# Kernel optimization log

Hardware: AMD Instinct MI355X
Metric: run time of the kernel (lower is better)

## Reference

```python
import jax, jax.numpy as jnp
import numpy as np

N = 50000          # nodes
E_RAND = 800000    # random edges
E = E_RAND + N     # + self loops -> 850000
F_IN = 256         # nembed
F_HID = 64         # nhid
H = 8              # nheads
NCLASS = 40
ALPHA = 0.2        # leakyrelu slope


def setup_inputs() -> dict:
    key = jax.random.key(0)
    ks = jax.random.split(key, 8)
    x = jax.random.normal(ks[0], (N, F_IN), dtype=jnp.float32)
    # random edges + self loops (guarantees every row-sum > 0, like adj + I)
    er = jax.random.randint(ks[1], (2, E_RAND), 0, N, dtype=jnp.int32)
    loops = jnp.tile(jnp.arange(N, dtype=jnp.int32)[None, :], (2, 1))
    edge_index = jnp.concatenate([er, loops], axis=1)  # [2, E]
    # per-head attention params (xavier-ish scale)
    W = jax.random.normal(ks[2], (H, F_IN, F_HID), dtype=jnp.float32) * (1.0 / np.sqrt(F_IN))
    a = jax.random.normal(ks[3], (H, 2 * F_HID), dtype=jnp.float32) * 0.1
    Wo = jax.random.normal(ks[4], (H * F_HID, F_HID), dtype=jnp.float32) * (1.0 / np.sqrt(H * F_HID))
    ao = jax.random.normal(ks[5], (2 * F_HID,), dtype=jnp.float32) * 0.1
    mlp_w = jax.random.normal(ks[6], (NCLASS, F_HID), dtype=jnp.float32) * 0.05
    mlp_b = jnp.zeros((NCLASS,), dtype=jnp.float32)
    return {"x": x, "edge_index": edge_index, "W": W, "a": a,
            "Wo": Wo, "ao": ao, "mlp_w": mlp_w, "mlp_b": mlp_b}


def _leaky(v):
    return jnp.where(v > 0, v, ALPHA * v)


def _spgat_layer(x, W, a, src, dst, n):
    """pyGAT SpGraphAttentionLayer (eval mode, dropout = identity).
    out[i] = sum_{e: src=i} exp(-leakyrelu(a.[h_src;h_dst])) * h[dst] / rowsum_i
    """
    h = x @ W                         # [N, D]
    D = W.shape[1]
    s_src = h @ a[:D]                 # [N]
    s_dst = h @ a[D:]                 # [N]
    # per-edge unnormalized attention (note the -exp(leaky) of original sp impl)
    e = jnp.exp(-_leaky(s_src[src] + s_dst[dst]))          # [E]
    rowsum = jax.ops.segment_sum(e, src, num_segments=n)   # [N]
    num = jax.ops.segment_sum(e[:, None] * h[dst], src, num_segments=n)  # [N, D]
    return num / rowsum[:, None]


def reference(x, edge_index, W, a, Wo, ao, mlp_w, mlp_b):
    src, dst = edge_index[0], edge_index[1]
    # multi-head attention, concat=True -> elu inside each head
    heads = [jax.nn.elu(_spgat_layer(x, W[i], a[i], src, dst, N)) for i in range(H)]
    xc = jnp.concatenate(heads, axis=1)                     # [N, H*F_HID]
    # dropout (eval) = identity
    xo = jax.nn.elu(_spgat_layer(xc, Wo, ao, src, dst, N))  # [N, F_HID]
    return xo @ mlp_w.T + mlp_b                             # [N, NCLASS]
```

## Files before the change

kernel.cpp:

```cpp
#include <hip/hip_runtime.h>

#define NN 50000
#define HH 8
#define ALPHA 0.2f
#define NPAD 50048

typedef short short8 __attribute__((ext_vector_type(8)));
typedef float f32x4 __attribute__((ext_vector_type(4)));

__device__ __forceinline__ float elu_f(float x) {
  return x > 0.f ? x : __expf(x) - 1.f;
}

__device__ __forceinline__ unsigned short f2bf(float f) {
  unsigned int u = __float_as_uint(f);
  unsigned int r = (u + 0x7fffu + ((u >> 16) & 1u)) >> 16;
  return (unsigned short)r;
}

__global__ void cvt_w_kernel(const float* __restrict__ W, unsigned short* __restrict__ Wt,
                             const float* __restrict__ Wo, unsigned short* __restrict__ Wot) {
  int tid = blockIdx.x * 256 + threadIdx.x;
  if (tid < HH * 256 * 64) {
    int h = tid / (256 * 64);
    int rem = tid - h * 256 * 64;
    int k = rem >> 6, c = rem & 63;
    Wt[((size_t)h * 64 + c) * 256 + k] = f2bf(W[tid]);
    return;
  }
  int t2 = tid - HH * 256 * 64;
  if (t2 < 512 * 64) {
    int k = t2 >> 6, c = t2 & 63;
    Wot[(size_t)c * 512 + k] = f2bf(Wo[t2]);
  }
}

__global__ void hist_kernel(const int* __restrict__ src, int* __restrict__ cnt, int E) {
  int e = blockIdx.x * blockDim.x + threadIdx.x;
  if (e < E) atomicAdd(&cnt[src[e]], 1);
}

__global__ __launch_bounds__(1024) void scan_blocks_kernel(const int* __restrict__ cnt,
    int* __restrict__ tmp, int* __restrict__ bsum, int n) {
  __shared__ int sh[1024];
  int i = blockIdx.x * 1024 + threadIdx.x;
  int v = (i < n) ? cnt[i] : 0;
  sh[threadIdx.x] = v;
  __syncthreads();
  for (int off = 1; off < 1024; off <<= 1) {
    int t = (threadIdx.x >= off) ? sh[threadIdx.x - off] : 0;
    __syncthreads();
    sh[threadIdx.x] += t;
    __syncthreads();
  }
  if (i < n) tmp[i] = sh[threadIdx.x] - v;
  if (threadIdx.x == 1023) bsum[blockIdx.x] = sh[1023];
}

__global__ __launch_bounds__(1024) void scan_apply_kernel(const int* __restrict__ tmp,
    const int* __restrict__ bsum, int* __restrict__ row_ptr, int* __restrict__ nxt,
    int n, int E, int nb) {
  __shared__ int boff_sh;
  if (threadIdx.x < 64) {
    int L = threadIdx.x;
    int v = (L < nb && L < (int)blockIdx.x) ? bsum[L] : 0;
#pragma unroll
    for (int off = 1; off < 64; off <<= 1) v += __shfl_xor(v, off, 64);
    if (L == 0) boff_sh = v;
  }
  __syncthreads();
  int i = blockIdx.x * 1024 + threadIdx.x;
  if (i < n) {
    int s = tmp[i] + boff_sh;
    row_ptr[i] = s;
    nxt[i] = s;
  }
  if (i == 0) row_ptr[n] = E;
}

__global__ void scatter_kernel(const int* __restrict__ src, const int* __restrict__ dst,
                               int* __restrict__ nxt, int* __restrict__ col, int E) {
  int e = blockIdx.x * blockDim.x + threadIdx.x;
  if (e < E) {
    int p = atomicAdd(&nxt[src[e]], 1);
    col[p] = dst[e];
  }
}

__global__ __launch_bounds__(256) void mfma_gemm1_kernel(
    const float* __restrict__ X, const unsigned short* __restrict__ Bt,
    const float* __restrict__ Aatt, unsigned short* __restrict__ Cout,
    float* __restrict__ ss, float* __restrict__ sd, int N) {
  __shared__ unsigned short Bs[64][264];
  unsigned short* stage = &Bs[0][0];
  int w = threadIdx.x >> 6, L = threadIdx.x & 63;
  int quad = L >> 4, l16 = L & 15;
  int m0 = blockIdx.x * 64;
  int myrow = m0 + w * 16 + l16;
  int rowc = min(myrow, N - 1);

  const float* Ar = X + (size_t)rowc * 256 + quad * 8;
  short8 areg[8];
#pragma unroll
  for (int ks = 0; ks < 8; ++ks) {
    float4 a0 = *(const float4*)(Ar + ks * 32);
    float4 a1 = *(const float4*)(Ar + ks * 32 + 4);
    areg[ks][0] = (short)f2bf(a0.x); areg[ks][1] = (short)f2bf(a0.y);
    areg[ks][2] = (short)f2bf(a0.z); areg[ks][3] = (short)f2bf(a0.w);
    areg[ks][4] = (short)f2bf(a1.x); areg[ks][5] = (short)f2bf(a1.y);
    areg[ks][6] = (short)f2bf(a1.z); areg[ks][7] = (short)f2bf(a1.w);
  }

  for (int y = 0; y < HH; ++y) {
    __syncthreads();
    {
      const unsigned short* Bsrc = Bt + (size_t)y * 64 * 256;
      for (int c = threadIdx.x; c < 2048; c += 256) {
        int n = c >> 5;
        int kq = (c & 31) << 3;
        *(uint4*)&Bs[n][kq] = *(const uint4*)(Bsrc + (size_t)n * 256 + kq);
      }
    }
    __syncthreads();

    f32x4 acc[4];
#pragma unroll
    for (int nt = 0; nt < 4; ++nt) acc[nt] = (f32x4)(0.f);
#pragma unroll
    for (int ks = 0; ks < 8; ++ks) {
#pragma unroll
      for (int nt = 0; nt < 4; ++nt) {
        short8 b = *(const short8*)&Bs[l16 + 16 * nt][ks * 32 + quad * 8];
        acc[nt] = __builtin_amdgcn_mfma_f32_16x16x32_bf16(areg[ks], b, acc[nt], 0, 0, 0);
      }
    }

    float as[4], ad[4];
#pragma unroll
    for (int nt = 0; nt < 4; ++nt) {
      as[nt] = Aatt[y * 128 + l16 + 16 * nt];
      ad[nt] = Aatt[y * 128 + 64 + l16 + 16 * nt];
    }
#pragma unroll
    for (int reg = 0; reg < 4; ++reg) {
      float p = 0.f, q = 0.f;
#pragma unroll
      for (int nt = 0; nt < 4; ++nt) {
        p += acc[nt][reg] * as[nt];
        q += acc[nt][reg] * ad[nt];
      }
#pragma unroll
      for (int off = 1; off < 16; off <<= 1) {
        p += __shfl_xor(p, off, 64);
        q += __shfl_xor(q, off, 64);
      }
      int row = m0 + w * 16 + quad * 4 + reg;
      if (l16 == 0 && row < N) {
        ss[(size_t)row * 8 + y] = p;
        sd[(size_t)row * 8 + y] = q;
      }
    }

    __syncthreads();
#pragma unroll
    for (int reg = 0; reg < 4; ++reg) {
      int lrow = w * 16 + quad * 4 + reg;
#pragma unroll
      for (int nt = 0; nt < 4; ++nt)
        stage[lrow * 72 + l16 + 16 * nt] = f2bf(acc[nt][reg]);
    }
    __syncthreads();
#pragma unroll
    for (int i = 0; i < 2; ++i) {
      int idx = threadIdx.x + 256 * i;
      int row = idx >> 3;
      int c8 = (idx & 7) << 3;
      if (m0 + row < N) {
        uint4 v = *(const uint4*)&stage[row * 72 + c8];
        *(uint4*)(Cout + ((size_t)(m0 + row)) * 512 + y * 64 + c8) = v;
      }
    }
  }
}

__global__ __launch_bounds__(256) void mfma_gemm2_kernel(
    const unsigned short* __restrict__ A, const unsigned short* __restrict__ Bt,
    const float* __restrict__ Aatt, unsigned short* __restrict__ Cout,
    float* __restrict__ ss, float* __restrict__ sd, int N) {
  __shared__ unsigned short Bs[64][520];
  unsigned short* stage = &Bs[0][0];
  {
    for (int c = threadIdx.x; c < 4096; c += 256) {
      int n = c >> 6;
      int kq = (c & 63) << 3;
      *(uint4*)&Bs[n][kq] = *(const uint4*)(Bt + (size_t)n * 512 + kq);
    }
  }
  __syncthreads();

  int w = threadIdx.x >> 6, L = threadIdx.x & 63;
  int quad = L >> 4, l16 = L & 15;
  int m0 = blockIdx.x * 64;
  int myrow = m0 + w * 16 + l16;
  const unsigned short* Ar = A + (size_t)myrow * 512 + quad * 8;

  f32x4 acc[4];
#pragma unroll
  for (int nt = 0; nt < 4; ++nt) acc[nt] = (f32x4)(0.f);

  short8 a_cur = *(const short8*)(Ar);
  for (int k0 = 0; k0 < 512; k0 += 32) {
    short8 a_nxt;
    if (k0 + 32 < 512) a_nxt = *(const short8*)(Ar + k0 + 32);
#pragma unroll
    for (int nt = 0; nt < 4; ++nt) {
      short8 b = *(const short8*)&Bs[l16 + 16 * nt][k0 + quad * 8];
      acc[nt] = __builtin_amdgcn_mfma_f32_16x16x32_bf16(a_cur, b, acc[nt], 0, 0, 0);
    }
    a_cur = a_nxt;
  }

  float as[4], ad[4];
#pragma unroll
  for (int nt = 0; nt < 4; ++nt) {
    as[nt] = Aatt[l16 + 16 * nt];
    ad[nt] = Aatt[64 + l16 + 16 * nt];
  }
#pragma unroll
  for (int reg = 0; reg < 4; ++reg) {
    float p = 0.f, q = 0.f;
#pragma unroll
    for (int nt = 0; nt < 4; ++nt) {
      p += acc[nt][reg] * as[nt];
      q += acc[nt][reg] * ad[nt];
    }
#pragma unroll
    for (int off = 1; off < 16; off <<= 1) {
      p += __shfl_xor(p, off, 64);
      q += __shfl_xor(q, off, 64);
    }
    int row = m0 + w * 16 + quad * 4 + reg;
    if (l16 == 0 && row < N) { ss[row] = p; sd[row] = q; }
  }

  __syncthreads();
#pragma unroll
  for (int reg = 0; reg < 4; ++reg) {
    int lrow = w * 16 + quad * 4 + reg;
#pragma unroll
    for (int nt = 0; nt < 4; ++nt)
      stage[lrow * 72 + l16 + 16 * nt] = f2bf(acc[nt][reg]);
  }
  __syncthreads();
#pragma unroll
  for (int i = 0; i < 2; ++i) {
    int idx = threadIdx.x + 256 * i;
    int row = idx >> 3;
    int c8 = (idx & 7) << 3;
    if (m0 + row < N) {
      uint4 v = *(const uint4*)&stage[row * 72 + c8];
      *(uint4*)(Cout + ((size_t)(m0 + row)) * 64 + c8) = v;
    }
  }
}

__global__ __launch_bounds__(256) void agg1_kernel(const unsigned short* __restrict__ table,
    const float* __restrict__ ss, const float* __restrict__ sd,
    const int* __restrict__ row_ptr, const int* __restrict__ col,
    unsigned short* __restrict__ xc, int N) {
  int bid = blockIdx.x;
  int r8 = bid & 7;
  int p = r8 >> 2;
  int nb = ((bid >> 3) << 2) | (r8 & 3);
  int wid = threadIdx.x >> 6, L = threadIdx.x & 63;
  int n = nb * 4 + wid;
  if (n >= N) return;
  int hq = L >> 4;
  int h = p * 4 + hq;
  int el = L & 15;
  float ssn = ss[n * 8 + h];
  int k0 = row_ptr[n], deg = row_ptr[n + 1] - k0;
  float acc[4] = {0.f, 0.f, 0.f, 0.f};
  float rs = 0.f;
  const char* tb = (const char*)table + p * 512;

  for (int c0 = 0; c0 < deg; c0 += 64) {
    int j = c0 + L;
    int d_l = (j < deg) ? col[k0 + j] : 0;
    int m = min(64, deg - c0);
    for (int g = 0; g < m; g += 16) {
      int eoff = g + el;
      int de = __shfl(d_l, eoff, 64);
      float s = ssn + sd[(size_t)de * 8 + h];
      float e = __expf(-fmaxf(s, ALPHA * s));
      if (eoff >= m) e = 0.f;
      rs += e;
      int gm = min(16, m - g);
      uint2 rv[16];
#pragma unroll
      for (int t = 0; t < 16; ++t) {
        if (t < gm) {
          int dg = __builtin_amdgcn_readlane(d_l, g + t);
          rv[t] = *(const uint2*)(tb + (size_t)dg * 1024 + L * 8);
        }
      }
#pragma unroll
      for (int t = 0; t < 16; ++t) {
        if (t < gm) {
          float ew = __shfl(e, (hq << 4) + t, 64);
          acc[0] += ew * __uint_as_float(rv[t].x << 16);
          acc[1] += ew * __uint_as_float(rv[t].x & 0xffff0000u);
          acc[2] += ew * __uint_as_float(rv[t].y << 16);
          acc[3] += ew * __uint_as_float(rv[t].y & 0xffff0000u);
        }
      }
    }
  }
  rs += __shfl_xor(rs, 1, 64);
  rs += __shfl_xor(rs, 2, 64);
  rs += __shfl_xor(rs, 4, 64);
  rs += __shfl_xor(rs, 8, 64);
  float inv = 1.f / rs;
  ushort4 pk;
  pk.x = f2bf(elu_f(acc[0] * inv));
  pk.y = f2bf(elu_f(acc[1] * inv));
  pk.z = f2bf(elu_f(acc[2] * inv));
  pk.w = f2bf(elu_f(acc[3] * inv));
  *(ushort4*)(xc + (size_t)n * 512 + p * 256 + L * 4) = pk;
}

__global__ __launch_bounds__(256) void agg2_final_kernel(const unsigned short* __restrict__ table,
    const float* __restrict__ ss, const float* __restrict__ sd,
    const int* __restrict__ row_ptr, const int* __restrict__ col,
    const float* __restrict__ mlp_w, const float* __restrict__ mlp_b,
    float* __restrict__ out, int N) {
  __shared__ float wsh[40 * 65];
  __shared__ float bsh[40];
  __shared__ float osh[4][68];
  for (int i = threadIdx.x; i < 40 * 64; i += 256) wsh[(i >> 6) * 65 + (i & 63)] = mlp_w[i];
  if (threadIdx.x < 40) bsh[threadIdx.x] = mlp_b[threadIdx.x];
  __syncthreads();

  int wid = threadIdx.x >> 6, L = threadIdx.x & 63;
  int n = blockIdx.x * 4 + wid;
  bool act = (n < N);
  float o = 0.f;
  if (act) {
    float ssn = ss[n];
    int k0 = row_ptr[n], deg = row_ptr[n + 1] - k0;
    float acc = 0.f, rs = 0.f;
    const char* base = (const char*)table;
    for (int c0 = 0; c0 < deg; c0 += 64) {
      int j = c0 + L;
      int d_l = 0;
      float e_l = 0.f;
      if (j < deg) {
        d_l = col[k0 + j];
        float s = ssn + sd[d_l];
        e_l = __expf(-fmaxf(s, ALPHA * s));
      }
      rs += e_l;
      int m = min(64, deg - c0);
      int off_l = d_l << 7;
      for (int g = 0; g < m; g += 8) {
        int gm = min(8, m - g);
        unsigned hv[8];
#pragma unroll
        for (int t = 0; t < 8; ++t) {
          if (t < gm) {
            int so = __builtin_amdgcn_readlane(off_l, g + t);
            hv[t] = *(const unsigned short*)(base + so + L * 2);
          }
        }
#pragma unroll
        for (int t = 0; t < 8; ++t) {
          if (t < gm) {
            float ew = __uint_as_float(
                (unsigned)__builtin_amdgcn_readlane(__float_as_uint(e_l), g + t));
            acc += ew * __uint_as_float(hv[t] << 16);
          }
        }
      }
    }
#pragma unroll
    for (int off = 1; off < 64; off <<= 1) rs += __shfl_xor(rs, off, 64);
    o = elu_f(acc / rs);
  }
  osh[wid][L] = o;
  __syncthreads();
  if (act && L < 40) {
    const float* wr = wsh + L * 65;
    const float* orow = osh[wid];
    float acc = bsh[L];
#pragma unroll
    for (int j = 0; j < 64; ++j) acc += orow[j] * wr[j];
    out[(size_t)n * 40 + L] = acc;
  }
}

extern "C" void kernel_launch(void* const* d_in, const int* in_sizes, int n_in,
                              void* d_out, int out_size, void* d_ws, size_t ws_size,
                              hipStream_t stream) {
  (void)n_in; (void)out_size; (void)ws_size;
  const float* x  = (const float*)d_in[0];
  const int*   ei = (const int*)d_in[1];
  const float* W  = (const float*)d_in[2];
  const float* a  = (const float*)d_in[3];
  const float* Wo = (const float*)d_in[4];
  const float* ao = (const float*)d_in[5];
  const float* mw = (const float*)d_in[6];
  const float* mb = (const float*)d_in[7];
  float* out = (float*)d_out;

  const int N = NN;
  const int E = in_sizes[1] / 2;
  const int* src = ei;
  const int* dst = ei + E;

  char* ws = (char*)d_ws;
  size_t off = 0;
  auto alloc = [&](size_t bytes) {
    char* p = ws + off;
    off = (off + bytes + 255) & ~(size_t)255;
    return p;
  };
  unsigned short* Wt  = (unsigned short*)alloc((size_t)HH * 64 * 256 * 2);
  unsigned short* Wot = (unsigned short*)alloc((size_t)64 * 512 * 2);
  unsigned short* h1b = (unsigned short*)alloc((size_t)N * 512 * 2);
  float* ss1     = (float*)alloc((size_t)N * 8 * 4);
  float* sd1     = (float*)alloc((size_t)N * 8 * 4);
  unsigned short* xc = (unsigned short*)alloc((size_t)NPAD * 512 * 2);
  unsigned short* h2b = (unsigned short*)alloc((size_t)N * 64 * 2);
  float* ss2     = (float*)alloc((size_t)N * 4);
  float* sd2     = (float*)alloc((size_t)N * 4);
  int*   row_ptr = (int*)  alloc((size_t)(N + 1) * 4);
  int*   nxt     = (int*)  alloc((size_t)N * 4);
  int*   cnt     = (int*)  alloc((size_t)N * 4);
  int*   tmp     = (int*)  alloc((size_t)N * 4);
  int*   bsum    = (int*)  alloc(64 * 4);
  int*   colv    = (int*)  alloc((size_t)E * 4);

  int eb = (E + 255) / 256;
  int nb1024 = (N + 1023) / 1024;

  hipLaunchKernelGGL(cvt_w_kernel, dim3((HH * 256 * 64 + 512 * 64 + 255) / 256), dim3(256),
                     0, stream, W, Wt, Wo, Wot);

  hipMemsetAsync(cnt, 0, (size_t)N * 4, stream);
  hipLaunchKernelGGL(hist_kernel, dim3(eb), dim3(256), 0, stream, src, cnt, E);
  hipLaunchKernelGGL(scan_blocks_kernel, dim3(nb1024), dim3(1024), 0, stream, cnt, tmp, bsum, N);
  hipLaunchKernelGGL(scan_apply_kernel, dim3(nb1024), dim3(1024), 0, stream,
                     tmp, bsum, row_ptr, nxt, N, E, nb1024);
  hipLaunchKernelGGL(scatter_kernel, dim3(eb), dim3(256), 0, stream, src, dst, nxt, colv, E);

  hipLaunchKernelGGL(mfma_gemm1_kernel, dim3(NPAD / 64), dim3(256), 0, stream,
                     x, Wt, a, h1b, ss1, sd1, N);
  hipLaunchKernelGGL(agg1_kernel, dim3(2 * ((N + 3) / 4)), dim3(256), 0, stream,
                     h1b, ss1, sd1, row_ptr, colv, xc, N);

  hipLaunchKernelGGL(mfma_gemm2_kernel, dim3(NPAD / 64), dim3(256), 0, stream,
                     xc, Wot, ao, h2b, ss2, sd2, N);
  hipLaunchKernelGGL(agg2_final_kernel, dim3((N + 3) / 4), dim3(256), 0, stream,
                     h2b, ss2, sd2, row_ptr, colv, mw, mb, out, N);
}
```

Before: 444.4 us.

## Pre-convert x to bf16 and retile GEMM1 as 128x128 block tiles

Adds a combined conversion kernel that writes x to a padded bf16 buffer and lays out W and Wo transposed in bf16. GEMM1 becomes a 2D-grid 128x128 tiled MFMA kernel with a k-loop through shared memory, each wave computing a 64x64 subtile of one head. The intent is higher MFMA density and register reuse per block. In exchange it adds an extra pass over x, drops the staged vectorized output stores for scattered 2-byte stores, and synchronizes every k-step.

Result: faster. 432.8 us (-2.6%).

```diff
diff --git a/kernel.cpp b/kernel.cpp
--- a/kernel.cpp
+++ b/kernel.cpp
@@ -18,20 +18,35 @@
   return (unsigned short)r;
 }
 
-__global__ void cvt_w_kernel(const float* __restrict__ W, unsigned short* __restrict__ Wt,
-                             const float* __restrict__ Wo, unsigned short* __restrict__ Wot) {
+__global__ void cvt_all_kernel(const float* __restrict__ x, unsigned short* __restrict__ xb,
+                               const float* __restrict__ W, unsigned short* __restrict__ Wtc,
+                               const float* __restrict__ Wo, unsigned short* __restrict__ Wot,
+                               int N) {
   int tid = blockIdx.x * 256 + threadIdx.x;
-  if (tid < HH * 256 * 64) {
-    int h = tid / (256 * 64);
-    int rem = tid - h * 256 * 64;
-    int k = rem >> 6, c = rem & 63;
-    Wt[((size_t)h * 64 + c) * 256 + k] = f2bf(W[tid]);
+  int n4x = NPAD * 64;
+  if (tid < n4x) {
+    int row = tid >> 6;
+    ushort4 o;
+    if (row < N) {
+      float4 v = ((const float4*)x)[tid];
+      o.x = f2bf(v.x); o.y = f2bf(v.y); o.z = f2bf(v.z); o.w = f2bf(v.w);
+    } else {
+      o.x = o.y = o.z = o.w = 0;
+    }
+    ((ushort4*)xb)[tid] = o;
     return;
   }
-  int t2 = tid - HH * 256 * 64;
-  if (t2 < 512 * 64) {
-    int k = t2 >> 6, c = t2 & 63;
-    Wot[(size_t)c * 512 + k] = f2bf(Wo[t2]);
+  int t1 = tid - n4x;
+  if (t1 < 512 * 256) {
+    int c = t1 >> 8, k = t1 & 255;
+    int h = c >> 6, cc = c & 63;
+    Wtc[t1] = f2bf(W[((size_t)h * 256 + k) * 64 + cc]);
+    return;
+  }
+  int t2 = t1 - 512 * 256;
+  if (t2 < 64 * 512) {
+    int c = t2 >> 9, k = t2 & 511;
+    Wot[t2] = f2bf(Wo[(size_t)k * 64 + c]);
   }
 }
 
@@ -88,96 +103,79 @@
 }
 
 __global__ __launch_bounds__(256) void mfma_gemm1_kernel(
-    const float* __restrict__ X, const unsigned short* __restrict__ Bt,
+    const unsigned short* __restrict__ A, const unsigned short* __restrict__ Wtc,
     const float* __restrict__ Aatt, unsigned short* __restrict__ Cout,
     float* __restrict__ ss, float* __restrict__ sd, int N) {
-  __shared__ unsigned short Bs[64][264];
-  unsigned short* stage = &Bs[0][0];
+  __shared__ unsigned short As[128][40];
+  __shared__ unsigned short Bs[128][40];
+  int m0 = blockIdx.x * 128;
+  int c0 = blockIdx.y * 128;
   int w = threadIdx.x >> 6, L = threadIdx.x & 63;
   int quad = L >> 4, l16 = L & 15;
-  int m0 = blockIdx.x * 64;
-  int myrow = m0 + w * 16 + l16;
-  int rowc = min(myrow, N - 1);
-
-  const float* Ar = X + (size_t)rowc * 256 + quad * 8;
-  short8 areg[8];
-#pragma unroll
-  for (int ks = 0; ks < 8; ++ks) {
-    float4 a0 = *(const float4*)(Ar + ks * 32);
-    float4 a1 = *(const float4*)(Ar + ks * 32 + 4);
-    areg[ks][0] = (short)f2bf(a0.x); areg[ks][1] = (short)f2bf(a0.y);
-    areg[ks][2] = (short)f2bf(a0.z); areg[ks][3] = (short)f2bf(a0.w);
-    areg[ks][4] = (short)f2bf(a1.x); areg[ks][5] = (short)f2bf(a1.y);
-    areg[ks][6] = (short)f2bf(a1.z); areg[ks][7] = (short)f2bf(a1.w);
-  }
-
-  for (int y = 0; y < HH; ++y) {
+  int wr = w >> 1, wc = w & 1;
+  int y = blockIdx.y * 2 + wc;
+
+  f32x4 acc[4][4];
+#pragma unroll
+  for (int mt = 0; mt < 4; ++mt)
+#pragma unroll
+    for (int nt = 0; nt < 4; ++nt) acc[mt][nt] = (f32x4)(0.f);
+
+  int sr0 = threadIdx.x >> 2;
+  int sk0 = (threadIdx.x & 3) << 3;
+
+  for (int k0 = 0; k0 < 256; k0 += 32) {
     __syncthreads();
-    {
-      const unsigned short* Bsrc = Bt + (size_t)y * 64 * 256;
-      for (int c = threadIdx.x; c < 2048; c += 256) {
-        int n = c >> 5;
-        int kq = (c & 31) << 3;
-        *(uint4*)&Bs[n][kq] = *(const uint4*)(Bsrc + (size_t)n * 256 + kq);
-      }
-    }
+    *(uint4*)&As[sr0][sk0]      = *(const uint4*)(A + (size_t)(m0 + sr0) * 256 + k0 + sk0);
+    *(uint4*)&As[sr0 + 64][sk0] = *(const uint4*)(A + (size_t)(m0 + sr0 + 64) * 256 + k0 + sk0);
+    *(uint4*)&Bs[sr0][sk0]      = *(const uint4*)(Wtc + (size_t)(c0 + sr0) * 256 + k0 + sk0);
+    *(uint4*)&Bs[sr0 + 64][sk0] = *(const uint4*)(Wtc + (size_t)(c0 + sr0 + 64) * 256 + k0 + sk0);
     __syncthreads();
 
-    f32x4 acc[4];
-#pragma unroll
-    for (int nt = 0; nt < 4; ++nt) acc[nt] = (f32x4)(0.f);
-#pragma unroll
-    for (int ks = 0; ks < 8; ++ks) {
+    short8 af[4], bf[4];
+#pragma unroll
+    for (int mt = 0; mt < 4; ++mt)
+      af[mt] = *(const short8*)&As[wr * 64 + mt * 16 + l16][quad * 8];
+#pragma unroll
+    for (int nt = 0; nt < 4; ++nt)
+      bf[nt] = *(const short8*)&Bs[wc * 64 + nt * 16 + l16][quad * 8];
+#pragma unroll
+    for (int mt = 0; mt < 4; ++mt)
+#pragma unroll
+      for (int nt = 0; nt < 4; ++nt)
+        acc[mt][nt] = __builtin_amdgcn_mfma_f32_16x16x32_bf16(af[mt], bf[nt], acc[mt][nt], 0, 0, 0);
+  }
+
+  float as[4], ad[4];
+#pragma unroll
+  for (int nt = 0; nt < 4; ++nt) {
+    as[nt] = Aatt[y * 128 + l16 + 16 * nt];
+    ad[nt] = Aatt[y * 128 + 64 + l16 + 16 * nt];
+  }
+#pragma unroll
+  for (int mt = 0; mt < 4; ++mt) {
+#pragma unroll
+    for (int reg = 0; reg < 4; ++reg) {
+      int row = m0 + wr * 64 + mt * 16 + quad * 4 + reg;
+      float p = 0.f, q = 0.f;
 #pragma unroll
       for (int nt = 0; nt < 4; ++nt) {
-        short8 b = *(const short8*)&Bs[l16 + 16 * nt][ks * 32 + quad * 8];
-        acc[nt] = __builtin_amdgcn_mfma_f32_16x16x32_bf16(areg[ks], b, acc[nt], 0, 0, 0);
-      }
-    }
-
-    float as[4], ad[4];
-#pragma unroll
-    for (int nt = 0; nt < 4; ++nt) {
-      as[nt] = Aatt[y * 128 + l16 + 16 * nt];
-      ad[nt] = Aatt[y * 128 + 64 + l16 + 16 * nt];
-    }
-#pragma unroll
-    for (int reg = 0; reg < 4; ++reg) {
-      float p = 0.f, q = 0.f;
-#pragma unroll
-      for (int nt = 0; nt < 4; ++nt) {
-        p += acc[nt][reg] * as[nt];
-        q += acc[nt][reg] * ad[nt];
+        p += acc[mt][nt][reg] * as[nt];
+        q += acc[mt][nt][reg] * ad[nt];
       }
 #pragma unroll
       for (int off = 1; off < 16; off <<= 1) {
         p += __shfl_xor(p, off, 64);
         q += __shfl_xor(q, off, 64);
       }
-      int row = m0 + w * 16 + quad * 4 + reg;
       if (l16 == 0 && row < N) {
         ss[(size_t)row * 8 + y] = p;
         sd[(size_t)row * 8 + y] = q;
       }
-    }
-
-    __syncthreads();
-#pragma unroll
-    for (int reg = 0; reg < 4; ++reg) {
-      int lrow = w * 16 + quad * 4 + reg;
-#pragma unroll
-      for (int nt = 0; nt < 4; ++nt)
-        stage[lrow * 72 + l16 + 16 * nt] = f2bf(acc[nt][reg]);
-    }
-    __syncthreads();
-#pragma unroll
-    for (int i = 0; i < 2; ++i) {
-      int idx = threadIdx.x + 256 * i;
-      int row = idx >> 3;
-      int c8 = (idx & 7) << 3;
-      if (m0 + row < N) {
-        uint4 v = *(const uint4*)&stage[row * 72 + c8];
-        *(uint4*)(Cout + ((size_t)(m0 + row)) * 512 + y * 64 + c8) = v;
+      if (row < N) {
+#pragma unroll
+        for (int nt = 0; nt < 4; ++nt)
+          Cout[(size_t)row * 512 + y * 64 + l16 + 16 * nt] = f2bf(acc[mt][nt][reg]);
       }
     }
   }
@@ -424,7 +422,8 @@
     off = (off + bytes + 255) & ~(size_t)255;
     return p;
   };
-  unsigned short* Wt  = (unsigned short*)alloc((size_t)HH * 64 * 256 * 2);
+  unsigned short* xb  = (unsigned short*)alloc((size_t)NPAD * 256 * 2);
+  unsigned short* Wtc = (unsigned short*)alloc((size_t)512 * 256 * 2);
   unsigned short* Wot = (unsigned short*)alloc((size_t)64 * 512 * 2);
   unsigned short* h1b = (unsigned short*)alloc((size_t)N * 512 * 2);
   float* ss1     = (float*)alloc((size_t)N * 8 * 4);
@@ -442,9 +441,10 @@
 
   int eb = (E + 255) / 256;
   int nb1024 = (N + 1023) / 1024;
-
-  hipLaunchKernelGGL(cvt_w_kernel, dim3((HH * 256 * 64 + 512 * 64 + 255) / 256), dim3(256),
-                     0, stream, W, Wt, Wo, Wot);
+  int cvt_total = NPAD * 64 + 512 * 256 + 64 * 512;
+
+  hipLaunchKernelGGL(cvt_all_kernel, dim3((cvt_total + 255) / 256), dim3(256), 0, stream,
+                     x, xb, W, Wtc, Wo, Wot, N);
 
   hipMemsetAsync(cnt, 0, (size_t)N * 4, stream);
   hipLaunchKernelGGL(hist_kernel, dim3(eb), dim3(256), 0, stream, src, cnt, E);
@@ -453,8 +453,8 @@
                      tmp, bsum, row_ptr, nxt, N, E, nb1024);
   hipLaunchKernelGGL(scatter_kernel, dim3(eb), dim3(256), 0, stream, src, dst, nxt, colv, E);
 
-  hipLaunchKernelGGL(mfma_gemm1_kernel, dim3(NPAD / 64), dim3(256), 0, stream,
-                     x, Wt, a, h1b, ss1, sd1, N);
+  hipLaunchKernelGGL(mfma_gemm1_kernel, dim3(NPAD / 128, 4), dim3(256), 0, stream,
+                     xb, Wtc, a, h1b, ss1, sd1, N);
   hipLaunchKernelGGL(agg1_kernel, dim3(2 * ((N + 3) / 4)), dim3(256), 0, stream,
                      h1b, ss1, sd1, row_ptr, colv, xc, N);
 
```
